# Performance work log

Measured on AMD Instinct MI355X. Metric: run time of the kernel, lower is better.

The kernel has to match this reference:

```python
import jax, jax.numpy as jnp
import numpy as np


def setup_inputs() -> dict:
    key = jax.random.key(0)
    k1, k2 = jax.random.split(key)
    B, C, H, W = 8, 64, 32, 32
    K = 8192
    x = jax.random.normal(k1, (B, C, H, W), dtype=jnp.float32)
    codebook = jax.random.normal(k2, (K, C), dtype=jnp.float32)
    return {"x": x, "codebook": codebook}


def reference(x, codebook):
    """Faithful JAX version of VQVAE.quantize().

    x:        [B, C, H, W] latent (output of pre_quant_conv)
    codebook: [K, C] embedding weight
    Returns (quant_out [B,C,H,W], commitment_loss, codebook_loss, indices [B,H,W]).
    """
    B, C, H, W = x.shape
    # [B, H, W, C] -> [B, N, C]
    xf = jnp.transpose(x, (0, 2, 3, 1)).reshape(B, H * W, C)

    # Squared pairwise distances (argmin of cdist == argmin of squared dist).
    x2 = jnp.sum(xf * xf, axis=-1, keepdims=True)            # [B, N, 1]
    e2 = jnp.sum(codebook * codebook, axis=-1)               # [K]
    xe = jnp.einsum('bnc,kc->bnk', xf, codebook)             # [B, N, K]
    d2 = x2 + e2[None, None, :] - 2.0 * xe                   # [B, N, K]
    idx = jnp.argmin(d2, axis=-1)                            # [B, N]

    quant = codebook[idx.reshape(-1)]                        # [B*N, C]
    xflat = xf.reshape(-1, C)                                # [B*N, C]

    commitment_loss = jnp.mean((jax.lax.stop_gradient(quant) - xflat) ** 2)
    codebook_loss = jnp.mean((quant - jax.lax.stop_gradient(xflat)) ** 2)

    # Straight-through estimator.
    quant_st = xflat + jax.lax.stop_gradient(quant - xflat)
    quant_out = jnp.transpose(quant_st.reshape(B, H, W, C), (0, 3, 1, 2))
    indices = idx.reshape(B, H, W)
    return quant_out, commitment_loss, codebook_loss, indices
```

## Files before the change

kernel.cpp:

```cpp
#include <hip/hip_runtime.h>


#define N_PTS   8192
#define K_CODES 8192
#define C_DIM   64
#define HWSZ    1024
#define QOUT_N  524288
#define SPLITS  32

#define WS_XS    0
#define WS_CBS   2097152
#define WS_E2H   4194304
#define WS_PACK  4227072
#define WS_PART  6324224

typedef __attribute__((ext_vector_type(8))) short    short8;
typedef __attribute__((ext_vector_type(8))) _Float16 half8;
typedef __attribute__((ext_vector_type(4))) float    floatx4;

__device__ __forceinline__ half8 as_h8(short8 v) {
    return __builtin_bit_cast(half8, v);
}
__device__ __forceinline__ void split2(float v, unsigned short& h,
                                       unsigned short& m) {
    _Float16 hh = (_Float16)v;
    float r = v - (float)hh;
    _Float16 mm = (_Float16)r;
    h = __builtin_bit_cast(unsigned short, hh);
    m = __builtin_bit_cast(unsigned short, mm);
}
__device__ __forceinline__ void cp16(const void* g, void* l) {
    __builtin_amdgcn_global_load_lds(
        (const __attribute__((address_space(1))) void*)g,
        (__attribute__((address_space(3))) void*)l, 16, 0, 0);
}
__device__ __forceinline__ void cp4(const void* g, void* l) {
    __builtin_amdgcn_global_load_lds(
        (const __attribute__((address_space(1))) void*)g,
        (__attribute__((address_space(3))) void*)l, 4, 0, 0);
}

__global__ __launch_bounds__(256)
void vq_prep_kernel(const float* __restrict__ x,
                    const float* __restrict__ cb,
                    unsigned short* __restrict__ xS,
                    unsigned short* __restrict__ cbS,
                    float* __restrict__ e2h)
{
    const int bx  = blockIdx.x;
    const int tid = threadIdx.x;

    if (bx < 32) {
        const int k = bx * 256 + tid;
        const float* row = cb + k * C_DIM;
        float s = 0.0f;
        #pragma unroll
        for (int g = 0; g < 8; ++g) {
            float4 a = *(const float4*)(row + g * 8);
            float4 b = *(const float4*)(row + g * 8 + 4);
            float vv[8] = {a.x, a.y, a.z, a.w, b.x, b.y, b.z, b.w};
            unsigned short h8[8], m8[8];
            #pragma unroll
            for (int j = 0; j < 8; ++j) {
                s = fmaf(vv[j], vv[j], s);
                split2(vv[j], h8[j], m8[j]);
            }
            *(uint4*)(cbS + ((size_t)(0 * 8 + g) * 8192 + k) * 8) = *(const uint4*)h8;
            *(uint4*)(cbS + ((size_t)(1 * 8 + g) * 8192 + k) * 8) = *(const uint4*)m8;
        }
        e2h[k] = 0.5f * s;
    } else {
        const int u = bx - 32;
        const int b = u >> 5, g = (u >> 2) & 7, q = u & 3;
        const int hw = q * 256 + tid;
        const float* xb = x + (size_t)(b * C_DIM + g * 8) * HWSZ + hw;
        unsigned short h8[8], m8[8];
        #pragma unroll
        for (int cq = 0; cq < 8; ++cq)
            split2(xb[cq * HWSZ], h8[cq], m8[cq]);
        const size_t n = (size_t)b * 1024 + hw;
        *(uint4*)(xS + ((size_t)(0 * 8 + g) * 8192 + n) * 8) = *(const uint4*)h8;
        *(uint4*)(xS + ((size_t)(1 * 8 + g) * 8192 + n) * 8) = *(const uint4*)m8;
    }
}

#define SEG_SHORTS 512
#define NSEGS      16
#define BUF_SHORTS 8320

__device__ __forceinline__ void computeTile(const half8 af[4][2][2],
                                            const unsigned short* __restrict__ bsrc,
                                            int tl, int quad, int col, int code,
                                            float bestv[4][4], int besti[4][4])
{
    half8 bf[2][2];
    #pragma unroll
    for (int p = 0; p < 2; ++p)
        #pragma unroll
        for (int s = 0; s < 2; ++s) {
            int seg = p * 8 + s * 4 + quad;
            bf[p][s] = as_h8(*(const short8*)(bsrc + seg * SEG_SHORTS + (tl * 16 + col) * 8));
        }
    float me2 = -((const float*)(bsrc + NSEGS * SEG_SHORTS))[tl * 16 + col];

    floatx4 acc[4];
    #pragma unroll
    for (int t = 0; t < 4; ++t) acc[t] = (floatx4){me2, me2, me2, me2};

    #pragma unroll
    for (int s = 0; s < 2; ++s) {
        #pragma unroll
        for (int t = 0; t < 4; ++t)
            acc[t] = __builtin_amdgcn_mfma_f32_16x16x32_f16(af[t][0][s], bf[0][s], acc[t], 0, 0, 0);
        #pragma unroll
        for (int t = 0; t < 4; ++t)
            acc[t] = __builtin_amdgcn_mfma_f32_16x16x32_f16(af[t][0][s], bf[1][s], acc[t], 0, 0, 0);
        #pragma unroll
        for (int t = 0; t < 4; ++t)
            acc[t] = __builtin_amdgcn_mfma_f32_16x16x32_f16(af[t][1][s], bf[0][s], acc[t], 0, 0, 0);
    }

    #pragma unroll
    for (int t = 0; t < 4; ++t)
        #pragma unroll
        for (int r = 0; r < 4; ++r) {
            float sc = acc[t][r];
            bool gt = sc > bestv[t][r];
            bestv[t][r] = gt ? sc   : bestv[t][r];
            besti[t][r] = gt ? code : besti[t][r];
        }
}

__global__ __launch_bounds__(256, 2)
void vq_argmin_kernel(const unsigned short* __restrict__ xS,
                      const unsigned short* __restrict__ cbS,
                      const float* __restrict__ e2h,
                      unsigned long long* __restrict__ packedS)
{
    __shared__ __align__(16) unsigned short sBuf[2][BUF_SHORTS];

    const int tid   = threadIdx.x;
    const int lane  = tid & 63;
    const int w     = tid >> 6;
    const int col   = lane & 15;
    const int quad  = lane >> 4;
    const int mb    = blockIdx.x;
    const int split = blockIdx.y;
    const int m0    = mb * 256 + w * 64;
    const int nb0   = split * 256;

    half8 af[4][2][2];
    #pragma unroll
    for (int t = 0; t < 4; ++t) {
        int pt = m0 + t * 16 + col;
        #pragma unroll
        for (int p = 0; p < 2; ++p)
            #pragma unroll
            for (int s = 0; s < 2; ++s) {
                int g = s * 4 + quad;
                af[t][p][s] = as_h8(*(const short8*)(xS + ((size_t)(p * 8 + g) * 8192 + pt) * 8));
            }
    }

    float bestv[4][4];
    int   besti[4][4];
    #pragma unroll
    for (int t = 0; t < 4; ++t)
        #pragma unroll
        for (int r = 0; r < 4; ++r) {
            bestv[t][r] = __uint_as_float(0xFF800000u);
            besti[t][r] = 0;
        }

    auto stage = [&](int k0, int buf) {
        unsigned short* dst = &sBuf[buf][0];
        #pragma unroll
        for (int i = 0; i < 4; ++i) {
            int f   = tid + i * 256;
            int seg = f >> 6;
            int l   = f & 63;
            cp16(cbS + ((size_t)seg * 8192 + k0 + l) * 8,
                 dst + seg * SEG_SHORTS + l * 8);
        }
        if (tid < 64)
            cp4(e2h + k0 + tid, (float*)(dst + NSEGS * SEG_SHORTS) + tid);
    };

    stage(nb0, 0);
    __syncthreads();

    for (int ch = 0; ch < 4; ++ch) {
        if (ch + 1 < 4) stage(nb0 + (ch + 1) * 64, (ch + 1) & 1);
        const unsigned short* bsrc = &sBuf[ch & 1][0];
        #pragma unroll
        for (int tl = 0; tl < 4; ++tl)
            computeTile(af, bsrc, tl, quad, col,
                        nb0 + ch * 64 + tl * 16 + col, bestv, besti);
        __syncthreads();
    }

    unsigned long long own = 0;
    #pragma unroll
    for (int t = 0; t < 4; ++t)
        #pragma unroll
        for (int r = 0; r < 4; ++r) {
            unsigned u = __float_as_uint(-bestv[t][r]);
            u = ((int)u < 0) ? ~u : (u | 0x80000000u);
            unsigned long long p = ((unsigned long long)u << 32) | (unsigned)besti[t][r];
            #pragma unroll
            for (int msk = 1; msk < 16; msk <<= 1) {
                unsigned long long q = __shfl_xor(p, msk, 64);
                p = (q < p) ? q : p;
            }
            own = (col == t * 4 + r) ? p : own;
        }
    const int mpt = m0 + (col >> 2) * 16 + quad * 4 + (col & 3);
    packedS[(size_t)split * N_PTS + mpt] = own;
}

__global__ __launch_bounds__(256)
void vq_gather_kernel(const float* __restrict__ x,
                      const float* __restrict__ cb,
                      const unsigned long long* __restrict__ packedS,
                      float* __restrict__ out,
                      float* __restrict__ part)
{
    __shared__ unsigned long long sred[8][32];
    const int tid = threadIdx.x;
    const int p   = tid & 31;
    const int sg  = tid >> 5;
    const int n0  = blockIdx.x * 32;
    const int n   = n0 + p;

    {
        unsigned long long v = packedS[(size_t)(sg * 4) * N_PTS + n];
        #pragma unroll
        for (int s = 1; s < 4; ++s) {
            unsigned long long q = packedS[(size_t)(sg * 4 + s) * N_PTS + n];
            v = (q < v) ? q : v;
        }
        sred[sg][p] = v;
    }
    __syncthreads();

    unsigned long long v = sred[0][p];
    #pragma unroll
    for (int s = 1; s < 8; ++s) {
        unsigned long long q = sred[s][p];
        v = (q < v) ? q : v;
    }
    const int idx = (int)(v & 0xFFFFFFFFull);
    if (tid < 32) out[QOUT_N + 2 + n0 + tid] = (float)idx;

    const int c0  = sg * 8;
    const int b   = n >> 10;
    const int hw  = n & 1023;
    const float* xb = x   + (size_t)b * (C_DIM * HWSZ) + hw;
    float*       ob = out + (size_t)b * (C_DIM * HWSZ) + hw;

    float s = 0.0f;
    #pragma unroll
    for (int c4 = 0; c4 < 2; ++c4) {
        float4 q = *(const float4*)(cb + (size_t)idx * C_DIM + c0 + c4 * 4);
        float qa[4] = {q.x, q.y, q.z, q.w};
        #pragma unroll
        for (int j = 0; j < 4; ++j) {
            int c = c0 + c4 * 4 + j;
            float xv = xb[c * HWSZ];
            float d  = qa[j] - xv;
            s = fmaf(d, d, s);
            ob[c * HWSZ] = xv + d;
        }
    }

    #pragma unroll
    for (int off = 32; off > 0; off >>= 1) s += __shfl_down(s, off, 64);
    if ((tid & 63) == 0) part[blockIdx.x * 4 + (tid >> 6)] = s;
}

__global__ __launch_bounds__(256)
void vq_final_kernel(const float* __restrict__ part, float* __restrict__ out)
{
    __shared__ float w[4];
    float s = part[threadIdx.x] + part[threadIdx.x + 256]
            + part[threadIdx.x + 512] + part[threadIdx.x + 768];
    #pragma unroll
    for (int off = 32; off > 0; off >>= 1) s += __shfl_down(s, off, 64);
    if ((threadIdx.x & 63) == 0) w[threadIdx.x >> 6] = s;
    __syncthreads();
    if (threadIdx.x == 0) {
        float m = (w[0] + w[1] + w[2] + w[3]) * (1.0f / (float)QOUT_N);
        out[QOUT_N]     = m;
        out[QOUT_N + 1] = m;
    }
}

extern "C" void kernel_launch(void* const* d_in, const int* in_sizes, int n_in,
                              void* d_out, int out_size, void* d_ws, size_t ws_size,
                              hipStream_t stream)
{
    const float* x  = (const float*)d_in[0];
    const float* cb = (const float*)d_in[1];
    float* out = (float*)d_out;
    char*  ws  = (char*)d_ws;
    (void)ws_size;

    unsigned short* xS  = (unsigned short*)(ws + WS_XS);
    unsigned short* cbS = (unsigned short*)(ws + WS_CBS);
    float* e2h = (float*)(ws + WS_E2H);
    unsigned long long* packedS = (unsigned long long*)(ws + WS_PACK);
    float* part = (float*)(ws + WS_PART);

    vq_prep_kernel<<<288, 256, 0, stream>>>(x, cb, xS, cbS, e2h);
    vq_argmin_kernel<<<dim3(N_PTS / 256, SPLITS), 256, 0, stream>>>(xS, cbS, e2h, packedS);
    vq_gather_kernel<<<256, 256, 0, stream>>>(x, cb, packedS, out, part);
    vq_final_kernel<<<1, 256, 0, stream>>>(part, out);
}
```

Baseline: 93.74 us.

## Double K-splits and stage whole codebook slice once, dropping the double buffer

```diff
diff --git a/kernel.cpp b/kernel.cpp
--- a/kernel.cpp
+++ b/kernel.cpp
@@ -6,13 +6,13 @@
 #define C_DIM   64
 #define HWSZ    1024
 #define QOUT_N  524288
-#define SPLITS  32
+#define SPLITS  64
 
 #define WS_XS    0
 #define WS_CBS   2097152
 #define WS_E2H   4194304
 #define WS_PACK  4227072
-#define WS_PART  6324224
+#define WS_PART  8421376
 
 typedef __attribute__((ext_vector_type(8))) short    short8;
 typedef __attribute__((ext_vector_type(8))) _Float16 half8;
@@ -84,13 +84,13 @@
     }
 }
 
-#define SEG_SHORTS 512
+#define SEG_SHORTS 1024
 #define NSEGS      16
-#define BUF_SHORTS 8320
+#define BUF_SHORTS 16640
 
 __device__ __forceinline__ void computeTile(const half8 af[4][2][2],
                                             const unsigned short* __restrict__ bsrc,
-                                            int tl, int quad, int col, int code,
+                                            int lc, int quad, int code,
                                             float bestv[4][4], int besti[4][4])
 {
     half8 bf[2][2];
@@ -99,9 +99,9 @@
         #pragma unroll
         for (int s = 0; s < 2; ++s) {
             int seg = p * 8 + s * 4 + quad;
-            bf[p][s] = as_h8(*(const short8*)(bsrc + seg * SEG_SHORTS + (tl * 16 + col) * 8));
-        }
-    float me2 = -((const float*)(bsrc + NSEGS * SEG_SHORTS))[tl * 16 + col];
+            bf[p][s] = as_h8(*(const short8*)(bsrc + seg * SEG_SHORTS + lc * 8));
+        }
+    float me2 = -((const float*)(bsrc + NSEGS * SEG_SHORTS))[lc];
 
     floatx4 acc[4];
     #pragma unroll
@@ -137,7 +137,7 @@
                       const float* __restrict__ e2h,
                       unsigned long long* __restrict__ packedS)
 {
-    __shared__ __align__(16) unsigned short sBuf[2][BUF_SHORTS];
+    __shared__ __align__(16) unsigned short sBuf[BUF_SHORTS];
 
     const int tid   = threadIdx.x;
     const int lane  = tid & 63;
@@ -147,7 +147,18 @@
     const int mb    = blockIdx.x;
     const int split = blockIdx.y;
     const int m0    = mb * 256 + w * 64;
-    const int nb0   = split * 256;
+    const int nb0   = split * 128;
+
+    #pragma unroll
+    for (int i = 0; i < 8; ++i) {
+        int f   = tid + i * 256;
+        int seg = f >> 7;
+        int l   = f & 127;
+        cp16(cbS + ((size_t)seg * 8192 + nb0 + l) * 8,
+             sBuf + seg * SEG_SHORTS + l * 8);
+    }
+    if (tid < 128)
+        cp4(e2h + nb0 + tid, (float*)(sBuf + NSEGS * SEG_SHORTS) + tid);
 
     half8 af[4][2][2];
     #pragma unroll
@@ -172,31 +183,15 @@
             besti[t][r] = 0;
         }
 
-    auto stage = [&](int k0, int buf) {
-        unsigned short* dst = &sBuf[buf][0];
-        #pragma unroll
-        for (int i = 0; i < 4; ++i) {
-            int f   = tid + i * 256;
-            int seg = f >> 6;
-            int l   = f & 63;
-            cp16(cbS + ((size_t)seg * 8192 + k0 + l) * 8,
-                 dst + seg * SEG_SHORTS + l * 8);
-        }
-        if (tid < 64)
-            cp4(e2h + k0 + tid, (float*)(dst + NSEGS * SEG_SHORTS) + tid);
-    };
-
-    stage(nb0, 0);
     __syncthreads();
 
-    for (int ch = 0; ch < 4; ++ch) {
-        if (ch + 1 < 4) stage(nb0 + (ch + 1) * 64, (ch + 1) & 1);
-        const unsigned short* bsrc = &sBuf[ch & 1][0];
-        #pragma unroll
-        for (int tl = 0; tl < 4; ++tl)
-            computeTile(af, bsrc, tl, quad, col,
-                        nb0 + ch * 64 + tl * 16 + col, bestv, besti);
-        __syncthreads();
+    #pragma unroll 1
+    for (int half = 0; half < 2; ++half) {
+        #pragma unroll
+        for (int tl = 0; tl < 4; ++tl) {
+            int lc = half * 64 + tl * 16 + col;
+            computeTile(af, sBuf, lc, quad, nb0 + lc, bestv, besti);
+        }
     }
 
     unsigned long long own = 0;
@@ -233,10 +228,10 @@
     const int n   = n0 + p;
 
     {
-        unsigned long long v = packedS[(size_t)(sg * 4) * N_PTS + n];
-        #pragma unroll
-        for (int s = 1; s < 4; ++s) {
-            unsigned long long q = packedS[(size_t)(sg * 4 + s) * N_PTS + n];
+        unsigned long long v = packedS[(size_t)(sg * 8) * N_PTS + n];
+        #pragma unroll
+        for (int s = 1; s < 8; ++s) {
+            unsigned long long q = packedS[(size_t)(sg * 8 + s) * N_PTS + n];
             v = (q < v) ? q : v;
         }
         sred[sg][p] = v;
```

Result: slower. 97.92 us (+4.5%).
